# Kernel tuning notes

Measured on AMD Instinct MI355X. Metric: run time of the kernel, lower is better.

Reference implementation:

```python
import jax, jax.numpy as jnp
import numpy as np

IMG, P, S, E, B = 224, 16, 8, 128, 64
N = (IMG - P) // S + 1          # patches per spatial dim (27)
L = N * N                       # num patches (729)
K = P * P                       # patch area (256)


def _flat_patch_idx():
    # flattened pixel index for each (patch, within-patch) element, shape [L, K]
    base = jnp.arange(N) * S            # top-left corner of each patch row/col
    off = jnp.arange(P)
    rows = base[:, None] + off[None, :]  # [N, P]
    hh = rows[:, None, :, None]          # [N,1,P,1]
    ww = rows[None, :, None, :]          # [1,N,1,P]
    return (hh * IMG + ww).reshape(L, K)  # row-major over patch positions, i*P+j within patch (matches torch Unfold)


def setup_inputs() -> dict:
    key = jax.random.key(0)
    k = jax.random.split(key, 5)
    x = jax.random.normal(k[0], (B, 3, IMG, IMG), dtype=jnp.float32)
    W_enc = jax.random.normal(k[1], (3, E, K), dtype=jnp.float32) * 0.02
    b_enc = jax.random.normal(k[2], (3, E), dtype=jnp.float32) * 0.02
    W_dec = jax.random.normal(k[3], (3, K, E), dtype=jnp.float32) * 0.02
    b_dec = jax.random.normal(k[4], (3, K), dtype=jnp.float32) * 0.02
    return {"x": x, "W_enc": W_enc, "b_enc": b_enc, "W_dec": W_dec, "b_dec": b_dec}


def reference(x, W_enc, b_enc, W_dec, b_dec):
    flat = _flat_patch_idx()                         # [L, K] int indices, static
    Bn = x.shape[0]
    # unfold: gather overlapping patches -> [B, 3, L, K]
    patches = x.reshape(Bn, 3, IMG * IMG)[:, :, flat]
    # per-channel linear encode: [B,3,L,E]
    emb = jnp.einsum('bclk,cek->bcle', patches, W_enc) + b_enc[:, None, :]
    # per-channel linear decode: [B,3,L,K]
    rec = jnp.einsum('bcle,cke->bclk', emb, W_dec) + b_dec[:, None, :]
    # fold: overlap-add scatter back to image
    fi = flat.reshape(-1)
    out = jnp.zeros((Bn, 3, IMG * IMG), x.dtype).at[:, :, fi].add(rec.reshape(Bn, 3, L * K))
    # normalization = fold(unfold(ones)) = per-pixel overlap count
    count = jnp.zeros((IMG * IMG,), x.dtype).at[fi].add(jnp.ones((L * K,), x.dtype))
    return (out / count).reshape(Bn, 3, IMG, IMG)
```

## Files before the change

### kernel.cpp

```cpp
#include <hip/hip_runtime.h>

#define IMG   224
#define IMG2  (IMG*IMG)
#define NN    27
#define KK    256
#define EE    128
#define NSTRIP 28
#define SCOLS 232
#define RSTR  132

typedef float f32x4 __attribute__((ext_vector_type(4)));
typedef short s16x8 __attribute__((ext_vector_type(8)));

__device__ __forceinline__ unsigned short f2bf(float f) {
    unsigned int u = __float_as_uint(f);
    u = (u + 0x7fffu + ((u >> 16) & 1u)) >> 16;
    return (unsigned short)u;
}
__device__ __forceinline__ float bf2f(unsigned short u) {
    return __uint_as_float((unsigned int)u << 16);
}
__device__ __forceinline__ uint2 pack4(f32x4 r) {
    uint2 u;
    asm("v_cvt_pk_bf16_f32 %0, %1, %2" : "=v"(u.x) : "v"(r.x), "v"(r.y));
    asm("v_cvt_pk_bf16_f32 %0, %1, %2" : "=v"(u.y) : "v"(r.z), "v"(r.w));
    return u;
}

__global__ void pack_M(const float* __restrict__ W_enc, const float* __restrict__ W_dec,
                       const float* __restrict__ b_enc, const float* __restrict__ b_dec,
                       unsigned short* __restrict__ APK, float* __restrict__ v) {
    int k = blockIdx.x, c = blockIdx.y, j = threadIdx.x;
    const float* wd = W_dec + ((size_t)c*KK + k)*EE;
    const float* we = W_enc + (size_t)c*EE*KK + j;
    float acc = 0.f;
    #pragma unroll 8
    for (int e = 0; e < EE; ++e) acc = fmaf(wd[e], we[(size_t)e*KK], acc);
    int kf = k >> 4, kr = k & 15, jb = j >> 5, g = (j >> 3) & 3, i = j & 7;
    APK[(size_t)c*65536 + (((kf*8 + jb)*64) + g*16 + kr)*8 + i] = f2bf(acc);

    __shared__ float pv[128];
    if (j < EE) pv[j] = wd[j] * b_enc[c*EE + j];
    __syncthreads();
    for (int off = 64; off > 0; off >>= 1) {
        if (j < off) pv[j] += pv[j + off];
        __syncthreads();
    }
    if (j == 0) v[c*KK + k] = pv[0] + b_dec[c*KK + k];
}

__global__ __launch_bounds__(256, 5)
void patch_ae_mfma(const float* __restrict__ x, const unsigned short* __restrict__ APK,
                   const float* __restrict__ v, float* __restrict__ out) {
    const int hid = blockIdx.x + NSTRIP*(blockIdx.y + 3*blockIdx.z);
    const int lid = (hid & 7)*672 + (hid >> 3);
    const int s  = lid % NSTRIP;
    const int t2 = lid / NSTRIP;
    const int c  = t2 % 3;
    const int b  = t2 / 3;

    const int tid  = threadIdx.x;
    const int lane = tid & 63, wave = tid >> 6;

    __shared__ __align__(16) unsigned short strip[24*SCOLS];
    __shared__ __align__(16) unsigned short rec[2][28][RSTR];
    __shared__ __align__(16) float vsh[256];

    vsh[tid] = v[c*256 + tid];

    const int prow    = wave >> 1;
    const int kq      = wave & 1;
    const int rowbase = prow ? 0 : 8;
    const int kfbase  = prow*8 + kq*4;
    const int g = lane >> 4, lr = lane & 15;
    const s16x8* APKc = (const s16x8*)(APK + (size_t)c*65536);

    s16x8 a0[4], a1[4];
    #pragma unroll
    for (int f = 0; f < 4; ++f) a0[f] = APKc[((kfbase + f)*8 + 0)*64 + lane];
    #pragma unroll
    for (int f = 0; f < 4; ++f) a1[f] = APKc[((kfbase + f)*8 + 1)*64 + lane];

    if (tid < 224) {
        const float* xb = x + (size_t)(b*3 + c)*IMG2;
        const int ybase = 8*s - 8;
        const int r0 = tid / 56;
        const int c4 = tid - r0*56;
        #pragma unroll
        for (int it = 0; it < 6; ++it) {
            int r  = r0 + it*4;
            int yr = ybase + r;
            float4 xv = make_float4(0.f, 0.f, 0.f, 0.f);
            if ((unsigned)yr < IMG)
                xv = ((const float4*)(xb + (size_t)yr*IMG))[c4];
            f32x4 xr = {xv.x, xv.y, xv.z, xv.w};
            *((uint2*)&strip[r*SCOLS + c4*4]) = pack4(xr);
        }
    }
    __syncthreads();

    {
        f32x4 acc[4][2];
        #pragma unroll
        for (int f = 0; f < 4; ++f)
            #pragma unroll
            for (int pf = 0; pf < 2; ++pf)
                acc[f][pf] = (f32x4){0.f, 0.f, 0.f, 0.f};

        const int c1 = (lr <= 10) ? (128 + 8*lr) : 208;

        #pragma unroll
        for (int jb = 0; jb < 8; ++jb) {
            const int jy  = 2*jb + (g >> 1);
            const int jx0 = (g & 1)*8;
            const unsigned short* srow = &strip[(rowbase + jy)*SCOLS + jx0];
            s16x8 bf0 = *((const s16x8*)&srow[8*lr]);
            s16x8 bf1 = *((const s16x8*)&srow[c1]);
            if ((jb & 1) == 0) {
                __builtin_amdgcn_s_setprio(1);
                #pragma unroll
                for (int f = 0; f < 4; ++f) {
                    acc[f][0] = __builtin_amdgcn_mfma_f32_16x16x32_bf16(a0[f], bf0, acc[f][0], 0, 0, 0);
                    acc[f][1] = __builtin_amdgcn_mfma_f32_16x16x32_bf16(a0[f], bf1, acc[f][1], 0, 0, 0);
                }
                __builtin_amdgcn_s_setprio(0);
                if (jb < 6) {
                    #pragma unroll
                    for (int f = 0; f < 4; ++f)
                        a0[f] = APKc[((kfbase + f)*8 + (jb+2))*64 + lane];
                }
            } else {
                __builtin_amdgcn_s_setprio(1);
                #pragma unroll
                for (int f = 0; f < 4; ++f) {
                    acc[f][0] = __builtin_amdgcn_mfma_f32_16x16x32_bf16(a1[f], bf0, acc[f][0], 0, 0, 0);
                    acc[f][1] = __builtin_amdgcn_mfma_f32_16x16x32_bf16(a1[f], bf1, acc[f][1], 0, 0, 0);
                }
                __builtin_amdgcn_s_setprio(0);
                if (jb < 6) {
                    #pragma unroll
                    for (int f = 0; f < 4; ++f)
                        a1[f] = APKc[((kfbase + f)*8 + (jb+2))*64 + lane];
                }
            }
        }

        #pragma unroll
        for (int f = 0; f < 4; ++f) {
            int klocal = kq*64 + f*16 + g*4;
            f32x4 bias = *((const f32x4*)&vsh[prow*128 + klocal]);
            #pragma unroll
            for (int pf = 0; pf < 2; ++pf) {
                f32x4 r = acc[f][pf] + bias;
                int p = min(pf*16 + lr, 27);
                *((uint2*)&rec[prow][p][klocal]) = pack4(r);
            }
        }
    }
    __syncthreads();

    if (tid < 224) {
        const int xc = tid;
        const int p1 = xc >> 3;
        const int v1 = (p1 <= NN-1);
        const int v0 = (p1 > 0);
        const int p0v = v0 ? p1 - 1 : 0;
        const int dx1 = xc & 7, dx0 = dx1 + 8;
        const int h0 = (s < NSTRIP-1);
        const int h1 = (s > 0);
        const int shift = (v0 & v1) + (h0 & h1);
        const float inv = __int_as_float(0x3f800000 - (shift << 23));
        float* orow = out + (size_t)(b*3 + c)*IMG2 + (size_t)(8*s)*IMG + xc;
        #pragma unroll
        for (int ry = 0; ry < 8; ++ry) {
            int kl1 = ry*16 + dx1, kl0 = ry*16 + dx0;
            float sum = 0.f;
            if (v1) {
                if (h0) sum += bf2f(rec[0][p1][kl1]);
                if (h1) sum += bf2f(rec[1][p1][kl1]);
            }
            if (v0) {
                if (h0) sum += bf2f(rec[0][p0v][kl0]);
                if (h1) sum += bf2f(rec[1][p0v][kl0]);
            }
            orow[(size_t)ry*IMG] = sum * inv;
        }
    }
}

extern "C" void kernel_launch(void* const* d_in, const int* in_sizes, int n_in,
                              void* d_out, int out_size, void* d_ws, size_t ws_size,
                              hipStream_t stream) {
    (void)in_sizes; (void)n_in; (void)out_size; (void)ws_size;
    const float* x     = (const float*)d_in[0];
    const float* W_enc = (const float*)d_in[1];
    const float* b_enc = (const float*)d_in[2];
    const float* W_dec = (const float*)d_in[3];
    const float* b_dec = (const float*)d_in[4];
    float* out = (float*)d_out;

    float*          v   = (float*)d_ws;
    unsigned short* APK = (unsigned short*)((char*)d_ws + 4096);

    pack_M<<<dim3(KK, 3), 256, 0, stream>>>(W_enc, W_dec, b_enc, b_dec, APK, v);
    patch_ae_mfma<<<dim3(NSTRIP, 3, 64), 256, 0, stream>>>(x, APK, v, out);
}
```

Baseline: 50.28 us.

## Process two batch images per block to reuse loaded weight fragments

```diff
diff --git a/kernel.cpp b/kernel.cpp
--- a/kernel.cpp
+++ b/kernel.cpp
@@ -49,20 +49,20 @@
     if (j == 0) v[c*KK + k] = pv[0] + b_dec[c*KK + k];
 }
 
-__global__ __launch_bounds__(256, 5)
+__global__ __launch_bounds__(256, 4)
 void patch_ae_mfma(const float* __restrict__ x, const unsigned short* __restrict__ APK,
                    const float* __restrict__ v, float* __restrict__ out) {
     const int hid = blockIdx.x + NSTRIP*(blockIdx.y + 3*blockIdx.z);
-    const int lid = (hid & 7)*672 + (hid >> 3);
+    const int lid = (hid & 7)*336 + (hid >> 3);
     const int s  = lid % NSTRIP;
     const int t2 = lid / NSTRIP;
     const int c  = t2 % 3;
-    const int b  = t2 / 3;
+    const int b0 = (t2 / 3) * 2;
 
     const int tid  = threadIdx.x;
     const int lane = tid & 63, wave = tid >> 6;
 
-    __shared__ __align__(16) unsigned short strip[24*SCOLS];
+    __shared__ __align__(16) unsigned short strip[2][24*SCOLS];
     __shared__ __align__(16) unsigned short rec[2][28][RSTR];
     __shared__ __align__(16) float vsh[256];
 
@@ -82,108 +82,122 @@
     for (int f = 0; f < 4; ++f) a1[f] = APKc[((kfbase + f)*8 + 1)*64 + lane];
 
     if (tid < 224) {
-        const float* xb = x + (size_t)(b*3 + c)*IMG2;
         const int ybase = 8*s - 8;
         const int r0 = tid / 56;
         const int c4 = tid - r0*56;
         #pragma unroll
-        for (int it = 0; it < 6; ++it) {
-            int r  = r0 + it*4;
-            int yr = ybase + r;
-            float4 xv = make_float4(0.f, 0.f, 0.f, 0.f);
-            if ((unsigned)yr < IMG)
-                xv = ((const float4*)(xb + (size_t)yr*IMG))[c4];
-            f32x4 xr = {xv.x, xv.y, xv.z, xv.w};
-            *((uint2*)&strip[r*SCOLS + c4*4]) = pack4(xr);
+        for (int img = 0; img < 2; ++img) {
+            const float* xb = x + (size_t)((b0 + img)*3 + c)*IMG2;
+            #pragma unroll
+            for (int it = 0; it < 6; ++it) {
+                int r  = r0 + it*4;
+                int yr = ybase + r;
+                float4 xv = make_float4(0.f, 0.f, 0.f, 0.f);
+                if ((unsigned)yr < IMG)
+                    xv = ((const float4*)(xb + (size_t)yr*IMG))[c4];
+                f32x4 xr = {xv.x, xv.y, xv.z, xv.w};
+                *((uint2*)&strip[img][r*SCOLS + c4*4]) = pack4(xr);
+            }
         }
     }
     __syncthreads();
 
-    {
-        f32x4 acc[4][2];
+    f32x4 acc[4][2][2];
+    #pragma unroll
+    for (int f = 0; f < 4; ++f)
         #pragma unroll
-        for (int f = 0; f < 4; ++f)
+        for (int im = 0; im < 2; ++im)
             #pragma unroll
             for (int pf = 0; pf < 2; ++pf)
-                acc[f][pf] = (f32x4){0.f, 0.f, 0.f, 0.f};
-
-        const int c1 = (lr <= 10) ? (128 + 8*lr) : 208;
-
-        #pragma unroll
-        for (int jb = 0; jb < 8; ++jb) {
-            const int jy  = 2*jb + (g >> 1);
-            const int jx0 = (g & 1)*8;
-            const unsigned short* srow = &strip[(rowbase + jy)*SCOLS + jx0];
-            s16x8 bf0 = *((const s16x8*)&srow[8*lr]);
-            s16x8 bf1 = *((const s16x8*)&srow[c1]);
-            if ((jb & 1) == 0) {
-                __builtin_amdgcn_s_setprio(1);
+                acc[f][im][pf] = (f32x4){0.f, 0.f, 0.f, 0.f};
+
+    const int c1 = (lr <= 10) ? (128 + 8*lr) : 208;
+
+    #pragma unroll
+    for (int jb = 0; jb < 8; ++jb) {
+        const int jy  = 2*jb + (g >> 1);
+        const int jx0 = (g & 1)*8;
+        const unsigned short* s0 = &strip[0][(rowbase + jy)*SCOLS + jx0];
+        const unsigned short* s1 = &strip[1][(rowbase + jy)*SCOLS + jx0];
+        s16x8 b00 = *((const s16x8*)&s0[8*lr]);
+        s16x8 b01 = *((const s16x8*)&s0[c1]);
+        s16x8 b10 = *((const s16x8*)&s1[8*lr]);
+        s16x8 b11 = *((const s16x8*)&s1[c1]);
+        if ((jb & 1) == 0) {
+            __builtin_amdgcn_s_setprio(1);
+            #pragma unroll
+            for (int f = 0; f < 4; ++f) {
+                acc[f][0][0] = __builtin_amdgcn_mfma_f32_16x16x32_bf16(a0[f], b00, acc[f][0][0], 0, 0, 0);
+                acc[f][0][1] = __builtin_amdgcn_mfma_f32_16x16x32_bf16(a0[f], b01, acc[f][0][1], 0, 0, 0);
+                acc[f][1][0] = __builtin_amdgcn_mfma_f32_16x16x32_bf16(a0[f], b10, acc[f][1][0], 0, 0, 0);
+                acc[f][1][1] = __builtin_amdgcn_mfma_f32_16x16x32_bf16(a0[f], b11, acc[f][1][1], 0, 0, 0);
+            }
+            __builtin_amdgcn_s_setprio(0);
+            if (jb < 6) {
                 #pragma unroll
-                for (int f = 0; f < 4; ++f) {
-                    acc[f][0] = __builtin_amdgcn_mfma_f32_16x16x32_bf16(a0[f], bf0, acc[f][0], 0, 0, 0);
-                    acc[f][1] = __builtin_amdgcn_mfma_f32_16x16x32_bf16(a0[f], bf1, acc[f][1], 0, 0, 0);
-                }
-                __builtin_amdgcn_s_setprio(0);
-                if (jb < 6) {
-                    #pragma unroll
-                    for (int f = 0; f < 4; ++f)
-                        a0[f] = APKc[((kfbase + f)*8 + (jb+2))*64 + lane];
-                }
-            } else {
-                __builtin_amdgcn_s_setprio(1);
+                for (int f = 0; f < 4; ++f)
+                    a0[f] = APKc[((kfbase + f)*8 + (jb+2))*64 + lane];
+            }
+        } else {
+            __builtin_amdgcn_s_setprio(1);
+            #pragma unroll
+            for (int f = 0; f < 4; ++f) {
+                acc[f][0][0] = __builtin_amdgcn_mfma_f32_16x16x32_bf16(a1[f], b00, acc[f][0][0], 0, 0, 0);
+                acc[f][0][1] = __builtin_amdgcn_mfma_f32_16x16x32_bf16(a1[f], b01, acc[f][0][1], 0, 0, 0);
+                acc[f][1][0] = __builtin_amdgcn_mfma_f32_16x16x32_bf16(a1[f], b10, acc[f][1][0], 0, 0, 0);
+                acc[f][1][1] = __builtin_amdgcn_mfma_f32_16x16x32_bf16(a1[f], b11, acc[f][1][1], 0, 0, 0);
+            }
+            __builtin_amdgcn_s_setprio(0);
+            if (jb < 6) {
                 #pragma unroll
-                for (int f = 0; f < 4; ++f) {
-                    acc[f][0] = __builtin_amdgcn_mfma_f32_16x16x32_bf16(a1[f], bf0, acc[f][0], 0, 0, 0);
-                    acc[f][1] = __builtin_amdgcn_mfma_f32_16x16x32_bf16(a1[f], bf1, acc[f][1], 0, 0, 0);
-                }
-                __builtin_amdgcn_s_setprio(0);
-                if (jb < 6) {
-                    #pragma unroll
-                    for (int f = 0; f < 4; ++f)
-                        a1[f] = APKc[((kfbase + f)*8 + (jb+2))*64 + lane];
-                }
-            }
-        }
-
+                for (int f = 0; f < 4; ++f)
+                    a1[f] = APKc[((kfbase + f)*8 + (jb+2))*64 + lane];
+            }
+        }
+    }
+
+    const int xc  = tid;
+    const int p1  = xc >> 3;
+    const int v1  = (p1 <= NN-1);
+    const int v0e = (p1 > 0);
+    const int p0v = v0e ? p1 - 1 : 0;
+    const int dx1 = xc & 7, dx0 = dx1 + 8;
+    const int h0  = (s < NSTRIP-1);
+    const int h1  = (s > 0);
+    const int shift = (v0e & v1) + (h0 & h1);
+    const float inv = __int_as_float(0x3f800000 - (shift << 23));
+
+    #pragma unroll
+    for (int img = 0; img < 2; ++img) {
+        __syncthreads();
         #pragma unroll
         for (int f = 0; f < 4; ++f) {
             int klocal = kq*64 + f*16 + g*4;
             f32x4 bias = *((const f32x4*)&vsh[prow*128 + klocal]);
             #pragma unroll
             for (int pf = 0; pf < 2; ++pf) {
-                f32x4 r = acc[f][pf] + bias;
+                f32x4 r = acc[f][img][pf] + bias;
                 int p = min(pf*16 + lr, 27);
                 *((uint2*)&rec[prow][p][klocal]) = pack4(r);
             }
         }
-    }
-    __syncthreads();
-
-    if (tid < 224) {
-        const int xc = tid;
-        const int p1 = xc >> 3;
-        const int v1 = (p1 <= NN-1);
-        const int v0 = (p1 > 0);
-        const int p0v = v0 ? p1 - 1 : 0;
-        const int dx1 = xc & 7, dx0 = dx1 + 8;
-        const int h0 = (s < NSTRIP-1);
-        const int h1 = (s > 0);
-        const int shift = (v0 & v1) + (h0 & h1);
-        const float inv = __int_as_float(0x3f800000 - (shift << 23));
-        float* orow = out + (size_t)(b*3 + c)*IMG2 + (size_t)(8*s)*IMG + xc;
-        #pragma unroll
-        for (int ry = 0; ry < 8; ++ry) {
-            int kl1 = ry*16 + dx1, kl0 = ry*16 + dx0;
-            float sum = 0.f;
-            if (v1) {
-                if (h0) sum += bf2f(rec[0][p1][kl1]);
-                if (h1) sum += bf2f(rec[1][p1][kl1]);
-            }
-            if (v0) {
-                if (h0) sum += bf2f(rec[0][p0v][kl0]);
-                if (h1) sum += bf2f(rec[1][p0v][kl0]);
-            }
-            orow[(size_t)ry*IMG] = sum * inv;
+        __syncthreads();
+        if (tid < 224) {
+            float* orow = out + (size_t)((b0 + img)*3 + c)*IMG2 + (size_t)(8*s)*IMG + xc;
+            #pragma unroll
+            for (int ry = 0; ry < 8; ++ry) {
+                int kl1 = ry*16 + dx1, kl0 = ry*16 + dx0;
+                float sum = 0.f;
+                if (v1) {
+                    if (h0) sum += bf2f(rec[0][p1][kl1]);
+                    if (h1) sum += bf2f(rec[1][p1][kl1]);
+                }
+                if (v0e) {
+                    if (h0) sum += bf2f(rec[0][p0v][kl0]);
+                    if (h1) sum += bf2f(rec[1][p0v][kl0]);
+                }
+                orow[(size_t)ry*IMG] = sum * inv;
+            }
         }
     }
 }
@@ -203,5 +217,5 @@
     unsigned short* APK = (unsigned short*)((char*)d_ws + 4096);
 
     pack_M<<<dim3(KK, 3), 256, 0, stream>>>(W_enc, W_dec, b_enc, b_dec, APK, v);
-    patch_ae_mfma<<<dim3(NSTRIP, 3, 64), 256, 0, stream>>>(x, APK, v, out);
-}
+    patch_ae_mfma<<<dim3(NSTRIP, 3, 32), 256, 0, stream>>>(x, APK, v, out);
+}
```

After: 54.88 us. 9.2% more time.
